# Optimization experiments

Measured on AMD Instinct MI355X. Metric: run time of the kernel, lower is better.

Reference implementation:

```python
import jax, jax.numpy as jnp
import numpy as np

NUM_CLASSES = 80
STRIDES = (8, 16, 32)
FEATS = ((80, 80), (40, 40), (20, 20))
RADIUS = 2.5
CAND_K = 10


def make_grids():
    grids, strides = [], []
    for (h, w), s in zip(FEATS, STRIDES):
        gx, gy = jnp.meshgrid(jnp.arange(w), jnp.arange(h))  # xy indexing: gx=col, gy=row
        g = jnp.stack([gx, gy], -1).reshape(-1, 2).astype(jnp.float32)
        grids.append(g)
        strides.append(jnp.full((h * w, 1), float(s), jnp.float32))
    return jnp.concatenate(grids, 0), jnp.concatenate(strides, 0)  # [A,2], [A,1]


def decode_level(p, s):
    # p: [B, 85, h, w] -> decoded [B, h*w, 85]; xy/wh decoded, conf/cls stay logits
    b, c, h, w = p.shape
    out = p.reshape(b, c, h * w).transpose(0, 2, 1)
    gx, gy = jnp.meshgrid(jnp.arange(w), jnp.arange(h))
    g = jnp.stack([gx, gy], -1).reshape(1, -1, 2).astype(p.dtype)
    xy = (out[..., :2] + g) * s
    wh = jnp.exp(out[..., 2:4]) * s
    return jnp.concatenate([xy, wh, out[..., 4:]], -1)


def pairwise_iou_cxcywh(a, b):
    # a: [G,4], b: [A,4] -> [G,A]
    tl = jnp.maximum(a[:, None, :2] - a[:, None, 2:] * 0.5, b[None, :, :2] - b[None, :, 2:] * 0.5)
    br = jnp.minimum(a[:, None, :2] + a[:, None, 2:] * 0.5, b[None, :, :2] + b[None, :, 2:] * 0.5)
    wh = jnp.clip(br - tl, 0.0)
    inter = wh[..., 0] * wh[..., 1]
    area_a = (a[:, 2] * a[:, 3])[:, None]
    area_b = (b[:, 2] * b[:, 3])[None, :]
    return inter / (area_a + area_b - inter + 1e-16)


def elem_iou_cxcywh(a, b):
    # a, b: [...,4] aligned -> [...]
    tl = jnp.maximum(a[..., :2] - a[..., 2:] * 0.5, b[..., :2] - b[..., 2:] * 0.5)
    br = jnp.minimum(a[..., :2] + a[..., 2:] * 0.5, b[..., :2] + b[..., 2:] * 0.5)
    wh = jnp.clip(br - tl, 0.0)
    inter = wh[..., 0] * wh[..., 1]
    area = a[..., 2] * a[..., 3] + b[..., 2] * b[..., 3]
    return inter / (area - inter + 1e-16)


def bce_logits(x, t):
    return jnp.maximum(x, 0.0) - x * t + jnp.log1p(jnp.exp(-jnp.abs(x)))


def assign_one(gt_b, gt_c, pbox, pconf, pcls, xy_center, stride_v):
    # SimOTA dynamic matching for one image. gt_b:[G,4], gt_c:[G], pbox:[A,4], pconf:[A,1], pcls:[A,C]
    G = gt_b.shape[0]
    # center-in-box / center-in-mirror(radius) masks
    bmin = gt_b[:, :2] - gt_b[:, 2:] * 0.5
    bmax = gt_b[:, :2] + gt_b[:, 2:] * 0.5
    d = jnp.concatenate([xy_center[None] - bmin[:, None], bmax[:, None] - xy_center[None]], -1)  # [G,A,4]
    in_box = jnp.min(d, -1) > 0.0
    mmin = gt_b[:, None, :2] - RADIUS * stride_v[None]
    mmax = gt_b[:, None, :2] + RADIUS * stride_v[None]
    d2 = jnp.concatenate([xy_center[None] - mmin, mmax - xy_center[None]], -1)
    in_mir = jnp.min(d2, -1) > 0.0
    union = jnp.any(in_box, 0) | jnp.any(in_mir, 0)  # [A]
    inter = in_box & in_mir  # [G,A]

    iou = pairwise_iou_cxcywh(gt_b, pbox)  # [G,A]
    iou_cost = -jnp.log(iou + 1e-8)
    # cls cost: BCE(sqrt(sigmoid(cls)*sigmoid(conf)), one_hot).sum(C), computed without [G,A,C]
    p = jnp.sqrt(jax.nn.sigmoid(pcls) * jax.nn.sigmoid(pconf))  # [A,C]
    logp = jnp.clip(jnp.log(jnp.clip(p, 1e-12)), -100.0)
    log1mp = jnp.clip(jnp.log(jnp.clip(1.0 - p, 1e-12)), -100.0)
    cls_cost = -(logp[:, gt_c].T - log1mp[:, gt_c].T + log1mp.sum(-1)[None, :])  # [G,A]

    cost = cls_cost + 3.0 * iou_cost + 1e5 * (~inter).astype(cost_dtype(pcls))
    cost = jnp.where(union[None, :], cost, 1e15)  # exclude anchors outside union (bool-index in torch)
    iou_m = jnp.where(union[None, :], iou, 0.0)

    # dynamic k per gt = clamp(int(sum top10 iou), 1)
    topk_iou, _ = jax.lax.top_k(iou_m, CAND_K)
    dyn_k = jnp.maximum(topk_iou.sum(1).astype(jnp.int32), 1)  # [G]
    _, idx = jax.lax.top_k(-cost, CAND_K)  # smallest-cost anchors per gt [G,10]
    valid = (jnp.arange(CAND_K)[None, :] < dyn_k[:, None]).astype(cost.dtype)
    mm = jnp.zeros_like(cost).at[jnp.arange(G)[:, None], idx].set(valid)  # [G,A]

    # resolve anchors matched to >1 gt by argmin cost
    multi = mm.sum(0) > 1.0
    best = jnp.argmin(cost, 0)  # [A]
    mm = jnp.where(multi[None, :], jax.nn.one_hot(best, G, dtype=mm.dtype).T, mm)

    fg = mm.sum(0) > 0.0  # [A]
    gt_idx = jnp.argmax(mm, 0)  # [A]
    match_iou = (mm * iou).sum(0)  # [A]
    return fg, gt_idx, match_iou


def cost_dtype(x):
    return x.dtype


def setup_inputs() -> dict:
    key = jax.random.key(0)
    ks = jax.random.split(key, 5)
    B, G = 32, 16
    p8 = jax.random.normal(ks[0], (B, 85, 80, 80), jnp.float32)
    p16 = jax.random.normal(ks[1], (B, 85, 40, 40), jnp.float32)
    p32 = jax.random.normal(ks[2], (B, 85, 20, 20), jnp.float32)
    u = jax.random.uniform(ks[3], (B, G, 4), jnp.float32)
    gt_boxes = jnp.concatenate([32.0 + u[..., :2] * 576.0, 16.0 + u[..., 2:] * 112.0], -1)
    gt_cls = jax.random.randint(ks[4], (B, G), 0, 80, dtype=jnp.int32)
    return {"p8": p8, "p16": p16, "p32": p32, "gt_boxes": gt_boxes, "gt_cls": gt_cls}


def reference(p8, p16, p32, gt_boxes, gt_cls):
    outs = [decode_level(p, s) for p, s in zip((p8, p16, p32), STRIDES)]
    outputs = jnp.concatenate(outs, 1)  # [B, 8400, 85]
    grids, stride_v = make_grids()
    xy_center = (grids + 0.5) * stride_v  # [A,2]
    pbox, pconf, pcls = outputs[..., :4], outputs[..., 4:5], outputs[..., 5:]

    sg = jax.lax.stop_gradient  # assignment is under torch.no_grad
    fg, gt_idx, match_iou = jax.vmap(assign_one, in_axes=(0, 0, 0, 0, 0, None, None))(
        gt_boxes, gt_cls, sg(pbox), sg(pconf), sg(pcls), xy_center, stride_v)
    match_iou = sg(match_iou)

    tgt_box = jnp.take_along_axis(gt_boxes, gt_idx[..., None], axis=1)  # [B,A,4]
    tgt_cls_id = jnp.take_along_axis(gt_cls, gt_idx, axis=1)  # [B,A]
    tgt_cls = jax.nn.one_hot(tgt_cls_id, NUM_CLASSES, dtype=outputs.dtype) * match_iou[..., None]
    fgf = fg.astype(outputs.dtype)

    iou_e = elem_iou_cxcywh(pbox, tgt_box)  # [B,A]
    loss_box = jnp.sum(fgf * (1.0 - iou_e ** 2))            # IOUloss, fg only
    loss_conf = jnp.sum(bce_logits(pconf[..., 0], fgf))     # all anchors
    loss_cls = jnp.sum(fgf[..., None] * bce_logits(pcls, tgt_cls))  # fg only
    n_fg = jnp.maximum(jnp.sum(fgf), 1.0)
    return (5.0 * loss_box + loss_conf + loss_cls) / n_fg
```

## Files before the change

### kernel.cpp

```cpp
#include <hip/hip_runtime.h>
#include <hip/hip_bf16.h>

#define A_TOT 8400
#define NB 32
#define NG 16
#define NC 80

#define K1_GX 132
#define NWAVE (K1_GX * NB * 4)
#define K3_CH 8
#define K3_W  1050

#define L2E 1.44269504088896340736f
#define LN2 0.69314718055994530942f

__device__ inline float fexp2(float x) { return __builtin_amdgcn_exp2f(x); }
__device__ inline float flog2(float x) { return __builtin_amdgcn_logf(x); }
__device__ inline float frcp(float x)  { return __builtin_amdgcn_rcpf(x); }
__device__ inline float fsqrtf_(float x) { return __builtin_amdgcn_sqrtf(x); }

__device__ inline float iou_cxcywh(float acx, float acy, float aw, float ah,
                                   float bcx, float bcy, float bw, float bh) {
    float tlx = fmaxf(acx - aw * 0.5f, bcx - bw * 0.5f);
    float tly = fmaxf(acy - ah * 0.5f, bcy - bh * 0.5f);
    float brx = fminf(acx + aw * 0.5f, bcx + bw * 0.5f);
    float bry = fminf(acy + ah * 0.5f, bcy + bh * 0.5f);
    float w = fmaxf(brx - tlx, 0.0f);
    float h = fmaxf(bry - tly, 0.0f);
    float inter = w * h;
    return inter / (aw * ah + bw * bh - inter + 1e-16f);
}

__device__ inline float dval_of(float x, float sc) {
    float u = fexp2(-x * L2E);
    float sx = frcp(1.0f + u);
    float pr = fsqrtf_(sx * sc);
    float lp  = fmaxf(LN2 * flog2(fmaxf(pr, 1e-12f)), -100.0f);
    float l1p = fmaxf(LN2 * flog2(fmaxf(1.0f - pr, 1e-12f)), -100.0f);
    return lp - l1p;
}

__device__ inline float cost_fast(float iou, float d, float sp, unsigned m, int g) {
    if (!((m >> 16) & 1u)) return 1e15f;
    float c = -(d + sp) - 3.0f * LN2 * flog2(iou + 1e-8f);
    if (!((m >> g) & 1u)) c += 100000.0f;
    return c;
}

__device__ inline unsigned long long umax64(unsigned long long a, unsigned long long b) {
    return a > b ? a : b;
}
__device__ inline unsigned long long umin64(unsigned long long a, unsigned long long b) {
    return a < b ? a : b;
}

__device__ inline const float* lvl_base(int a, int b, const float* p8, const float* p16,
                                        const float* p32, int& hw, int& HW, int& W, float& s) {
    if (a < 6400) { hw = a;        HW = 6400; W = 80; s = 8.0f;  return p8  + (size_t)b * 85 * 6400; }
    if (a < 8000) { hw = a - 6400; HW = 1600; W = 40; s = 16.0f; return p16 + (size_t)b * 85 * 1600; }
    { hw = a - 8000; HW = 400; W = 20; s = 32.0f; return p32 + (size_t)b * 85 * 400; }
}

__global__ __launch_bounds__(256) void k1_decode(
    const float* __restrict__ p8, const float* __restrict__ p16, const float* __restrict__ p32,
    const float* __restrict__ gtb,
    float4* __restrict__ pbox, float* __restrict__ sl1p,
    float* __restrict__ s0cls, float* __restrict__ confw, float* __restrict__ ssc,
    unsigned* __restrict__ umask, float* __restrict__ part) {
    int b = blockIdx.y;
    int tid = threadIdx.x;
    int a = blockIdx.x * 64 + (tid >> 2);
    int quad = tid & 3;
    float bce0_conf = 0.0f;
    if (a < A_TOT) {
        int hw, HW, W;
        float s;
        const float* base = lvl_base(a, b, p8, p16, p32, hw, HW, W, s);

        float cf = base[4 * HW + hw];
        float uc = fexp2(-cf * L2E);
        float suc = 1.0f + uc;
        float sc = frcp(suc);

        const float* cbase = base + (5 + quad * 20) * HW + hw;
        float x[20];
#pragma unroll
        for (int j = 0; j < 20; j++) x[j] = cbase[j * HW];
        float s0 = 0.0f, suml1p = 0.0f;
#pragma unroll
        for (int j = 0; j < 20; j++) {
            float u = fexp2(-x[j] * L2E);
            float su = 1.0f + u;
            s0 += x[j] + LN2 * flog2(su);
            float pr = fsqrtf_(frcp(su) * sc);
            suml1p += fmaxf(LN2 * flog2(fmaxf(1.0f - pr, 1e-12f)), -100.0f);
        }
        s0 += __shfl_xor(s0, 1, 64);
        s0 += __shfl_xor(s0, 2, 64);
        suml1p += __shfl_xor(suml1p, 1, 64);
        suml1p += __shfl_xor(suml1p, 2, 64);

        if (quad == 0) {
            float tx = base[hw], ty = base[HW + hw];
            float tw = base[2 * HW + hw], th = base[3 * HW + hw];
            int gx = hw % W, gy = hw / W;
            float pcx = (tx + (float)gx) * s;
            float pcy = (ty + (float)gy) * s;
            float pw = fexp2(tw * L2E) * s;
            float ph = fexp2(th * L2E) * s;

            bce0_conf = cf + LN2 * flog2(suc);

            float xc = ((float)gx + 0.5f) * s;
            float yc = ((float)gy + 0.5f) * s;
            unsigned m = 0;
            bool uni = false;
            float r = 2.5f * s;
#pragma unroll 4
            for (int g = 0; g < NG; g++) {
                float gcx = gtb[(b * NG + g) * 4 + 0];
                float gcy = gtb[(b * NG + g) * 4 + 1];
                float gw  = gtb[(b * NG + g) * 4 + 2];
                float gh  = gtb[(b * NG + g) * 4 + 3];
                bool ib = (xc > gcx - gw * 0.5f) && (gcx + gw * 0.5f > xc) &&
                          (yc > gcy - gh * 0.5f) && (gcy + gh * 0.5f > yc);
                bool im = (xc > gcx - r) && (gcx + r > xc) &&
                          (yc > gcy - r) && (gcy + r > yc);
                uni |= (ib || im);
                if (ib && im) m |= (1u << g);
            }
            if (uni) m |= (1u << 16);

            size_t i = (size_t)b * A_TOT + a;
            pbox[i] = make_float4(pcx, pcy, pw, ph);
            confw[i] = cf;
            ssc[i] = sc;
            sl1p[i] = suml1p;
            s0cls[i] = s0;
            umask[i] = m;
        }
    }
    float v = bce0_conf;
    for (int off = 32; off; off >>= 1) v += __shfl_down(v, off, 64);
    if ((tid & 63) == 0) {
        int wave = (blockIdx.y * gridDim.x + blockIdx.x) * 4 + (tid >> 6);
        part[wave] = v;
    }
}

__global__ __launch_bounds__(512, 4) void k2_assign(
    const float* __restrict__ gtb, const int* __restrict__ gtc,
    const float4* __restrict__ pbox, const float* __restrict__ sl1p,
    const float* __restrict__ ssc, const unsigned* __restrict__ umask,
    const float* __restrict__ p8, const float* __restrict__ p16, const float* __restrict__ p32,
    int* __restrict__ sel, int* __restrict__ nsel) {
    __shared__ unsigned long long wred[8];
    int blk = blockIdx.x;
    int b = blk >> 4, g = blk & 15;
    int tid = threadIdx.x;

    float gcx = gtb[blk * 4 + 0], gcy = gtb[blk * 4 + 1];
    float gw = gtb[blk * 4 + 2],  gh = gtb[blk * 4 + 3];
    int cg = gtc[blk];

    unsigned long long topI[10];
    unsigned long long topC[10];
#pragma unroll
    for (int i = 0; i < 10; i++) { topI[i] = 0ull; topC[i] = 0xFFFFFFFFFFFFFFFFull; }

    for (int a = tid; a < A_TOT; a += 512) {
        size_t i = (size_t)b * A_TOT + a;
        float4 pb = pbox[i];
        unsigned m = umask[i];
        float iou = iou_cxcywh(gcx, gcy, gw, gh, pb.x, pb.y, pb.z, pb.w);

        float cost = 1e15f;
        float mi = 0.0f;
        if ((m >> 16) & 1u) {
            mi = iou;
            int hw, HW, W;
            float s;
            const float* base = lvl_base(a, b, p8, p16, p32, hw, HW, W, s);
            float x = base[(5 + cg) * HW + hw];
            float d = dval_of(x, ssc[i]);
            cost = -(d + sl1p[i]) - 3.0f * LN2 * flog2(iou + 1e-8f);
            if (!((m >> g) & 1u)) cost += 100000.0f;
        }

        if (mi > 0.0f) {
            unsigned long long kI = ((unsigned long long)__float_as_uint(mi) << 32) | (unsigned)a;
            if (kI > topI[9]) {
                unsigned long long v = kI;
#pragma unroll
                for (int i2 = 0; i2 < 10; i2++) {
                    unsigned long long big = umax64(topI[i2], v);
                    v = umin64(topI[i2], v);
                    topI[i2] = big;
                }
            }
        }
        unsigned long long kC = ((unsigned long long)__float_as_uint(cost) << 32) | (unsigned)a;
        if (kC < topC[9]) {
            unsigned long long v = kC;
#pragma unroll
            for (int i2 = 0; i2 < 10; i2++) {
                unsigned long long sml = umin64(topC[i2], v);
                v = umax64(topC[i2], v);
                topC[i2] = sml;
            }
        }
    }

    float ksum = 0.0f;
    for (int rr = 0; rr < 10; rr++) {
        unsigned long long h = topI[0];
        for (int off = 32; off; off >>= 1) h = umax64(h, __shfl_xor(h, off, 64));
        if ((tid & 63) == 0) wred[tid >> 6] = h;
        __syncthreads();
        unsigned long long w = wred[0];
#pragma unroll
        for (int j = 1; j < 8; j++) w = umax64(w, wred[j]);
        ksum += __uint_as_float((unsigned)(w >> 32));
        if (topI[0] == w) {
#pragma unroll
            for (int i = 0; i < 9; i++) topI[i] = topI[i + 1];
            topI[9] = 0ull;
        }
        __syncthreads();
    }
    int dynk = (int)ksum;
    if (dynk < 1) dynk = 1;
    if (dynk > 10) dynk = 10;

    for (int rr = 0; rr < 10; rr++) {
        unsigned long long h = topC[0];
        for (int off = 32; off; off >>= 1) h = umin64(h, __shfl_xor(h, off, 64));
        if ((tid & 63) == 0) wred[tid >> 6] = h;
        __syncthreads();
        unsigned long long w = wred[0];
#pragma unroll
        for (int j = 1; j < 8; j++) w = umin64(w, wred[j]);
        if (tid == 0) sel[blk * 10 + rr] = (int)(w & 0xffffffffu);
        if (topC[0] == w) {
#pragma unroll
            for (int i = 0; i < 9; i++) topC[i] = topC[i + 1];
            topC[9] = 0xFFFFFFFFFFFFFFFFull;
        }
        __syncthreads();
    }
    if (tid == 0) nsel[blk] = dynk;
}

__global__ __launch_bounds__(256) void k3_resolve(
    const float* __restrict__ gtb, const int* __restrict__ gtc,
    const float4* __restrict__ pbox, const float* __restrict__ sl1p,
    const unsigned* __restrict__ umask,
    const float* __restrict__ confw, const float* __restrict__ ssc,
    const float* __restrict__ s0cls,
    const int* __restrict__ sel, const int* __restrict__ nsel,
    const float* __restrict__ p8, const float* __restrict__ p16, const float* __restrict__ p32,
    float4* __restrict__ part3) {
    __shared__ unsigned tag[K3_W];
    __shared__ float gb[NG * 4];
    __shared__ int gc[NG];
    __shared__ float red[256];
    int b = blockIdx.y, chunk = blockIdx.x, tid = threadIdx.x;
    int a0 = chunk * K3_W;

    for (int j = tid; j < K3_W; j += 256) tag[j] = 0;
    if (tid < NG * 4) gb[tid] = gtb[b * NG * 4 + tid];
    if (tid < NG) gc[tid] = gtc[b * NG + tid];
    __syncthreads();

    if (tid < NG * 10) {
        int g = tid / 10, k = tid % 10;
        if (k < nsel[b * NG + g]) {
            int a = sel[(b * NG + g) * 10 + k];
            if (a >= a0 && a < a0 + K3_W)
                atomicAdd(&tag[a - a0], 0x10000u + (unsigned)(g + 1));
        }
    }
    __syncthreads();

    float lbox = 0.0f, lconfc = 0.0f, lcls = 0.0f, nfg = 0.0f;
    for (int j = tid; j < K3_W; j += 256) {
        unsigned t = tag[j];
        unsigned cnt = t >> 16;
        if (!cnt) continue;
        int a = a0 + j;
        size_t i = (size_t)b * A_TOT + a;
        float4 pb = pbox[i];
        int hw, HW, W;
        float s;
        const float* base = lvl_base(a, b, p8, p16, p32, hw, HW, W, s);
        int gs;
        if (cnt == 1) {
            gs = (int)(t & 0xffffu) - 1;
        } else {
            unsigned m = umask[i];
            float sp = sl1p[i];
            float sc = ssc[i];
            float bc = 3.402823466e38f;
            gs = 0;
            for (int g = 0; g < NG; g++) {
                float iou = iou_cxcywh(gb[g * 4], gb[g * 4 + 1], gb[g * 4 + 2], gb[g * 4 + 3],
                                       pb.x, pb.y, pb.z, pb.w);
                float x = base[(5 + gc[g]) * HW + hw];
                float d = dval_of(x, sc);
                float c = cost_fast(iou, d, sp, m, g);
                if (c < bc) { bc = c; gs = g; }
            }
        }
        float miou = iou_cxcywh(gb[gs * 4], gb[gs * 4 + 1], gb[gs * 4 + 2], gb[gs * 4 + 3],
                                pb.x, pb.y, pb.z, pb.w);
        int cid = gc[gs];
        float xcid = base[(5 + cid) * HW + hw];

        lbox += 1.0f - miou * miou;
        lconfc -= confw[i];
        lcls += s0cls[i] - xcid * miou;
        nfg += 1.0f;
    }

    float vals[4] = {lbox, lconfc, lcls, nfg};
    float outv[4];
    for (int i = 0; i < 4; i++) {
        red[tid] = vals[i];
        __syncthreads();
        for (int s2 = 128; s2 > 0; s2 >>= 1) {
            if (tid < s2) red[tid] += red[tid + s2];
            __syncthreads();
        }
        outv[i] = red[0];
        __syncthreads();
    }
    if (tid == 0)
        part3[blockIdx.y * K3_CH + chunk] = make_float4(outv[0], outv[1], outv[2], outv[3]);
}

__global__ __launch_bounds__(256) void k4_final(
    const float* __restrict__ part, const float4* __restrict__ part3, float* __restrict__ out) {
    __shared__ float red[256];
    int tid = threadIdx.x;
    float v = 0.0f;
    for (int i = tid; i < NWAVE; i += 256) v += part[i];
    float4 p = part3[tid & 255];
    float vals[5] = {v, p.x, p.y, p.z, p.w};
    float tot[5];
    for (int i = 0; i < 5; i++) {
        red[tid] = vals[i];
        __syncthreads();
        for (int s2 = 128; s2 > 0; s2 >>= 1) {
            if (tid < s2) red[tid] += red[tid + s2];
            __syncthreads();
        }
        tot[i] = red[0];
        __syncthreads();
    }
    if (tid == 0) {
        float nfg = tot[4];
        if (nfg < 1.0f) nfg = 1.0f;
        out[0] = (5.0f * tot[1] + (tot[0] + tot[2]) + tot[3]) / nfg;
    }
}

extern "C" void kernel_launch(void* const* d_in, const int* in_sizes, int n_in,
                              void* d_out, int out_size, void* d_ws, size_t ws_size,
                              hipStream_t stream) {
    const float* p8  = (const float*)d_in[0];
    const float* p16 = (const float*)d_in[1];
    const float* p32 = (const float*)d_in[2];
    const float* gtb = (const float*)d_in[3];
    const int*   gtc = (const int*)d_in[4];

    char* w = (char*)d_ws;
    float4* pbox = (float4*)w;                 w += (size_t)NB * A_TOT * sizeof(float4);
    float* sl1p  = (float*)w;                  w += (size_t)NB * A_TOT * sizeof(float);
    float* s0c   = (float*)w;                  w += (size_t)NB * A_TOT * sizeof(float);
    float* conf  = (float*)w;                  w += (size_t)NB * A_TOT * sizeof(float);
    float* sscp  = (float*)w;                  w += (size_t)NB * A_TOT * sizeof(float);
    unsigned* um = (unsigned*)w;               w += (size_t)NB * A_TOT * sizeof(unsigned);
    int* sel     = (int*)w;                    w += (size_t)NB * NG * 10 * sizeof(int);
    int* nsel    = (int*)w;                    w += (size_t)NB * NG * sizeof(int);
    float* part  = (float*)w;                  w += (size_t)NWAVE * sizeof(float);
    float4* part3 = (float4*)w;                w += (size_t)NB * K3_CH * sizeof(float4);

    k1_decode<<<dim3(K1_GX, NB), 256, 0, stream>>>(
        p8, p16, p32, gtb, pbox, sl1p, s0c, conf, sscp, um, part);
    k2_assign<<<NB * NG, 512, 0, stream>>>(gtb, gtc, pbox, sl1p, sscp, um,
                                           p8, p16, p32, sel, nsel);
    k3_resolve<<<dim3(K3_CH, NB), 256, 0, stream>>>(gtb, gtc, pbox, sl1p, um, conf, sscp, s0c,
                                                    sel, nsel, p8, p16, p32, part3);
    k4_final<<<1, 256, 0, stream>>>(part, part3, (float*)d_out);
}
```

Baseline: 195.3 us.

## Skip class reads for anchors outside all GT regions and pack per-anchor records

k1 now runs one thread per anchor and reads the 80 class logits only when the anchor falls inside some GT box or radius region, which cuts most of the heavy input traffic and transcendental math. The sum of class BCE terms (s0) moves from k1 into k3, where it is computed only for foreground anchors. Mask, sigmoid confidence, log(1-p) sum and conf logit are packed into a single float4 record, replacing five separate scalar arrays so k2 and k3 each do one vector load. In exchange, k1 threads are divergent and each does serial 80-element loops with less parallelism per anchor, and k3 does extra per-foreground work.

```diff
diff --git a/kernel.cpp b/kernel.cpp
--- a/kernel.cpp
+++ b/kernel.cpp
@@ -6,7 +6,7 @@
 #define NG 16
 #define NC 80
 
-#define K1_GX 132
+#define K1_GX 33
 #define NWAVE (K1_GX * NB * 4)
 #define K3_CH 8
 #define K3_W  1050
@@ -64,81 +64,70 @@
 __global__ __launch_bounds__(256) void k1_decode(
     const float* __restrict__ p8, const float* __restrict__ p16, const float* __restrict__ p32,
     const float* __restrict__ gtb,
-    float4* __restrict__ pbox, float* __restrict__ sl1p,
-    float* __restrict__ s0cls, float* __restrict__ confw, float* __restrict__ ssc,
-    unsigned* __restrict__ umask, float* __restrict__ part) {
+    float4* __restrict__ pbox, float4* __restrict__ rec, float* __restrict__ part) {
     int b = blockIdx.y;
     int tid = threadIdx.x;
-    int a = blockIdx.x * 64 + (tid >> 2);
-    int quad = tid & 3;
+    int a = blockIdx.x * 256 + tid;
     float bce0_conf = 0.0f;
     if (a < A_TOT) {
         int hw, HW, W;
         float s;
         const float* base = lvl_base(a, b, p8, p16, p32, hw, HW, W, s);
 
+        float tx = base[hw], ty = base[HW + hw];
+        float tw = base[2 * HW + hw], th = base[3 * HW + hw];
         float cf = base[4 * HW + hw];
+        int gx = hw % W, gy = hw / W;
+        float pcx = (tx + (float)gx) * s;
+        float pcy = (ty + (float)gy) * s;
+        float pw = fexp2(tw * L2E) * s;
+        float ph = fexp2(th * L2E) * s;
+
         float uc = fexp2(-cf * L2E);
         float suc = 1.0f + uc;
         float sc = frcp(suc);
-
-        const float* cbase = base + (5 + quad * 20) * HW + hw;
-        float x[20];
-#pragma unroll
-        for (int j = 0; j < 20; j++) x[j] = cbase[j * HW];
-        float s0 = 0.0f, suml1p = 0.0f;
-#pragma unroll
-        for (int j = 0; j < 20; j++) {
-            float u = fexp2(-x[j] * L2E);
-            float su = 1.0f + u;
-            s0 += x[j] + LN2 * flog2(su);
-            float pr = fsqrtf_(frcp(su) * sc);
-            suml1p += fmaxf(LN2 * flog2(fmaxf(1.0f - pr, 1e-12f)), -100.0f);
-        }
-        s0 += __shfl_xor(s0, 1, 64);
-        s0 += __shfl_xor(s0, 2, 64);
-        suml1p += __shfl_xor(suml1p, 1, 64);
-        suml1p += __shfl_xor(suml1p, 2, 64);
-
-        if (quad == 0) {
-            float tx = base[hw], ty = base[HW + hw];
-            float tw = base[2 * HW + hw], th = base[3 * HW + hw];
-            int gx = hw % W, gy = hw / W;
-            float pcx = (tx + (float)gx) * s;
-            float pcy = (ty + (float)gy) * s;
-            float pw = fexp2(tw * L2E) * s;
-            float ph = fexp2(th * L2E) * s;
-
-            bce0_conf = cf + LN2 * flog2(suc);
-
-            float xc = ((float)gx + 0.5f) * s;
-            float yc = ((float)gy + 0.5f) * s;
-            unsigned m = 0;
-            bool uni = false;
-            float r = 2.5f * s;
+        bce0_conf = cf + LN2 * flog2(suc);
+
+        float xc = ((float)gx + 0.5f) * s;
+        float yc = ((float)gy + 0.5f) * s;
+        unsigned m = 0;
+        bool uni = false;
+        float r = 2.5f * s;
 #pragma unroll 4
-            for (int g = 0; g < NG; g++) {
-                float gcx = gtb[(b * NG + g) * 4 + 0];
-                float gcy = gtb[(b * NG + g) * 4 + 1];
-                float gw  = gtb[(b * NG + g) * 4 + 2];
-                float gh  = gtb[(b * NG + g) * 4 + 3];
-                bool ib = (xc > gcx - gw * 0.5f) && (gcx + gw * 0.5f > xc) &&
-                          (yc > gcy - gh * 0.5f) && (gcy + gh * 0.5f > yc);
-                bool im = (xc > gcx - r) && (gcx + r > xc) &&
-                          (yc > gcy - r) && (gcy + r > yc);
-                uni |= (ib || im);
-                if (ib && im) m |= (1u << g);
-            }
-            if (uni) m |= (1u << 16);
-
-            size_t i = (size_t)b * A_TOT + a;
-            pbox[i] = make_float4(pcx, pcy, pw, ph);
-            confw[i] = cf;
-            ssc[i] = sc;
-            sl1p[i] = suml1p;
-            s0cls[i] = s0;
-            umask[i] = m;
-        }
+        for (int g = 0; g < NG; g++) {
+            float gcx = gtb[(b * NG + g) * 4 + 0];
+            float gcy = gtb[(b * NG + g) * 4 + 1];
+            float gw  = gtb[(b * NG + g) * 4 + 2];
+            float gh  = gtb[(b * NG + g) * 4 + 3];
+            bool ib = (xc > gcx - gw * 0.5f) && (gcx + gw * 0.5f > xc) &&
+                      (yc > gcy - gh * 0.5f) && (gcy + gh * 0.5f > yc);
+            bool im = (xc > gcx - r) && (gcx + r > xc) &&
+                      (yc > gcy - r) && (gcy + r > yc);
+            uni |= (ib || im);
+            if (ib && im) m |= (1u << g);
+        }
+        if (uni) m |= (1u << 16);
+
+        float suml1p = 0.0f;
+        if (uni) {
+            const float* cbase = base + 5 * HW + hw;
+#pragma unroll
+            for (int cc = 0; cc < NC; cc += 20) {
+                float x[20];
+#pragma unroll
+                for (int j = 0; j < 20; j++) x[j] = cbase[(cc + j) * HW];
+#pragma unroll
+                for (int j = 0; j < 20; j++) {
+                    float u = fexp2(-x[j] * L2E);
+                    float pr = fsqrtf_(frcp(1.0f + u) * sc);
+                    suml1p += fmaxf(LN2 * flog2(fmaxf(1.0f - pr, 1e-12f)), -100.0f);
+                }
+            }
+        }
+
+        size_t i = (size_t)b * A_TOT + a;
+        pbox[i] = make_float4(pcx, pcy, pw, ph);
+        rec[i] = make_float4(__uint_as_float(m), sc, suml1p, cf);
     }
     float v = bce0_conf;
     for (int off = 32; off; off >>= 1) v += __shfl_down(v, off, 64);
@@ -150,8 +139,7 @@
 
 __global__ __launch_bounds__(512, 4) void k2_assign(
     const float* __restrict__ gtb, const int* __restrict__ gtc,
-    const float4* __restrict__ pbox, const float* __restrict__ sl1p,
-    const float* __restrict__ ssc, const unsigned* __restrict__ umask,
+    const float4* __restrict__ pbox, const float4* __restrict__ rec,
     const float* __restrict__ p8, const float* __restrict__ p16, const float* __restrict__ p32,
     int* __restrict__ sel, int* __restrict__ nsel) {
     __shared__ unsigned long long wred[8];
@@ -171,7 +159,8 @@
     for (int a = tid; a < A_TOT; a += 512) {
         size_t i = (size_t)b * A_TOT + a;
         float4 pb = pbox[i];
-        unsigned m = umask[i];
+        float4 rc = rec[i];
+        unsigned m = __float_as_uint(rc.x);
         float iou = iou_cxcywh(gcx, gcy, gw, gh, pb.x, pb.y, pb.z, pb.w);
 
         float cost = 1e15f;
@@ -182,8 +171,8 @@
             float s;
             const float* base = lvl_base(a, b, p8, p16, p32, hw, HW, W, s);
             float x = base[(5 + cg) * HW + hw];
-            float d = dval_of(x, ssc[i]);
-            cost = -(d + sl1p[i]) - 3.0f * LN2 * flog2(iou + 1e-8f);
+            float d = dval_of(x, rc.y);
+            cost = -(d + rc.z) - 3.0f * LN2 * flog2(iou + 1e-8f);
             if (!((m >> g) & 1u)) cost += 100000.0f;
         }
 
@@ -253,10 +242,7 @@
 
 __global__ __launch_bounds__(256) void k3_resolve(
     const float* __restrict__ gtb, const int* __restrict__ gtc,
-    const float4* __restrict__ pbox, const float* __restrict__ sl1p,
-    const unsigned* __restrict__ umask,
-    const float* __restrict__ confw, const float* __restrict__ ssc,
-    const float* __restrict__ s0cls,
+    const float4* __restrict__ pbox, const float4* __restrict__ rec,
     const int* __restrict__ sel, const int* __restrict__ nsel,
     const float* __restrict__ p8, const float* __restrict__ p16, const float* __restrict__ p32,
     float4* __restrict__ part3) {
@@ -290,6 +276,7 @@
         int a = a0 + j;
         size_t i = (size_t)b * A_TOT + a;
         float4 pb = pbox[i];
+        float4 rc = rec[i];
         int hw, HW, W;
         float s;
         const float* base = lvl_base(a, b, p8, p16, p32, hw, HW, W, s);
@@ -297,17 +284,15 @@
         if (cnt == 1) {
             gs = (int)(t & 0xffffu) - 1;
         } else {
-            unsigned m = umask[i];
-            float sp = sl1p[i];
-            float sc = ssc[i];
+            unsigned m = __float_as_uint(rc.x);
             float bc = 3.402823466e38f;
             gs = 0;
             for (int g = 0; g < NG; g++) {
                 float iou = iou_cxcywh(gb[g * 4], gb[g * 4 + 1], gb[g * 4 + 2], gb[g * 4 + 3],
                                        pb.x, pb.y, pb.z, pb.w);
                 float x = base[(5 + gc[g]) * HW + hw];
-                float d = dval_of(x, sc);
-                float c = cost_fast(iou, d, sp, m, g);
+                float d = dval_of(x, rc.y);
+                float c = cost_fast(iou, d, rc.z, m, g);
                 if (c < bc) { bc = c; gs = g; }
             }
         }
@@ -316,9 +301,23 @@
         int cid = gc[gs];
         float xcid = base[(5 + cid) * HW + hw];
 
+        float s0 = 0.0f;
+        const float* cbase = base + 5 * HW + hw;
+#pragma unroll
+        for (int cc = 0; cc < NC; cc += 20) {
+            float x[20];
+#pragma unroll
+            for (int jj = 0; jj < 20; jj++) x[jj] = cbase[(cc + jj) * HW];
+#pragma unroll
+            for (int jj = 0; jj < 20; jj++) {
+                float u = fexp2(-x[jj] * L2E);
+                s0 += x[jj] + LN2 * flog2(1.0f + u);
+            }
+        }
+
         lbox += 1.0f - miou * miou;
-        lconfc -= confw[i];
-        lcls += s0cls[i] - xcid * miou;
+        lconfc -= rc.w;
+        lcls += s0 - xcid * miou;
         nfg += 1.0f;
     }
 
@@ -375,21 +374,17 @@
 
     char* w = (char*)d_ws;
     float4* pbox = (float4*)w;                 w += (size_t)NB * A_TOT * sizeof(float4);
-    float* sl1p  = (float*)w;                  w += (size_t)NB * A_TOT * sizeof(float);
-    float* s0c   = (float*)w;                  w += (size_t)NB * A_TOT * sizeof(float);
-    float* conf  = (float*)w;                  w += (size_t)NB * A_TOT * sizeof(float);
-    float* sscp  = (float*)w;                  w += (size_t)NB * A_TOT * sizeof(float);
-    unsigned* um = (unsigned*)w;               w += (size_t)NB * A_TOT * sizeof(unsigned);
+    float4* rec  = (float4*)w;                 w += (size_t)NB * A_TOT * sizeof(float4);
     int* sel     = (int*)w;                    w += (size_t)NB * NG * 10 * sizeof(int);
     int* nsel    = (int*)w;                    w += (size_t)NB * NG * sizeof(int);
     float* part  = (float*)w;                  w += (size_t)NWAVE * sizeof(float);
     float4* part3 = (float4*)w;                w += (size_t)NB * K3_CH * sizeof(float4);
 
     k1_decode<<<dim3(K1_GX, NB), 256, 0, stream>>>(
-        p8, p16, p32, gtb, pbox, sl1p, s0c, conf, sscp, um, part);
-    k2_assign<<<NB * NG, 512, 0, stream>>>(gtb, gtc, pbox, sl1p, sscp, um,
+        p8, p16, p32, gtb, pbox, rec, part);
+    k2_assign<<<NB * NG, 512, 0, stream>>>(gtb, gtc, pbox, rec,
                                            p8, p16, p32, sel, nsel);
-    k3_resolve<<<dim3(K3_CH, NB), 256, 0, stream>>>(gtb, gtc, pbox, sl1p, um, conf, sscp, s0c,
+    k3_resolve<<<dim3(K3_CH, NB), 256, 0, stream>>>(gtb, gtc, pbox, rec,
                                                     sel, nsel, p8, p16, p32, part3);
     k4_final<<<1, 256, 0, stream>>>(part, part3, (float*)d_out);
 }
```

New measurement: 185.8 us. 4.9% less time.
